# Kernel tuning notes

Hardware: AMD Instinct MI355X
Metric: run time of the kernel (lower is better)

## Reference

```python
import jax, jax.numpy as jnp
import numpy as np
from jax import lax

B, T, V, E, H, C = 16, 1024, 256, 512, 1024, 256


def lstm_layer(x, h0, c0, Wih, Whh, bih, bhh):
    """Single unidirectional LSTM layer, batch_first. x: (B,T,I). Returns (ys,(h,c)).
    Torch gate order: i, f, g, o. Input projection hoisted out of the scan (one big GEMM)."""
    xg = jnp.einsum('bti,gi->btg', x, Wih) + (bih + bhh)  # (B,T,4H)

    def step(carry, xt):
        h, c = carry
        gates = xt + h @ Whh.T
        i, f, g, o = jnp.split(gates, 4, axis=-1)
        c = jax.nn.sigmoid(f) * c + jax.nn.sigmoid(i) * jnp.tanh(g)
        h = jax.nn.sigmoid(o) * jnp.tanh(c)
        return (h, c), h

    (h, c), ys = lax.scan(step, (h0, c0), jnp.swapaxes(xg, 0, 1))
    return jnp.swapaxes(ys, 0, 1), h, c


def run_stack(emb_tokens, h0s, c0s, layers):
    """layers: list of (Wih, Whh, bih, bhh). h0s/c0s: (L,B,H)."""
    x = emb_tokens
    hs, cs = [], []
    for l, (Wih, Whh, bih, bhh) in enumerate(layers):
        x, h, c = lstm_layer(x, h0s[l], c0s[l], Wih, Whh, bih, bhh)
        hs.append(h)
        cs.append(c)
    return x, jnp.stack(hs), jnp.stack(cs)


def setup_inputs() -> dict:
    key = jax.random.key(0)
    ks = iter(jax.random.split(key, 32))
    s = 1.0 / np.sqrt(H)

    def u(shape):
        return jax.random.uniform(next(ks), shape, jnp.float32, -s, s)

    inp = {"x": jax.random.randint(next(ks), (B, T), 0, V)}
    inp["enc_emb"] = jax.random.normal(next(ks), (V, E), jnp.float32)
    inp["dec_emb"] = jax.random.normal(next(ks), (V, E), jnp.float32)
    for pre in ("enc", "dec"):
        for l in range(2):
            I = E if l == 0 else H
            inp[f"{pre}_Wih{l}"] = u((4 * H, I))
            inp[f"{pre}_Whh{l}"] = u((4 * H, H))
            inp[f"{pre}_bih{l}"] = u((4 * H,))
            inp[f"{pre}_bhh{l}"] = u((4 * H,))
    inp["out_W"] = u((C, H))
    inp["out_b"] = u((C,))
    return inp


def reference(x, enc_emb, dec_emb,
              enc_Wih0, enc_Whh0, enc_bih0, enc_bhh0,
              enc_Wih1, enc_Whh1, enc_bih1, enc_bhh1,
              dec_Wih0, dec_Whh0, dec_bih0, dec_bhh0,
              dec_Wih1, dec_Whh1, dec_bih1, dec_bhh1,
              out_W, out_b):
    enc_layers = [(enc_Wih0, enc_Whh0, enc_bih0, enc_bhh0),
                  (enc_Wih1, enc_Whh1, enc_bih1, enc_bhh1)]
    dec_layers = [(dec_Wih0, dec_Whh0, dec_bih0, dec_bhh0),
                  (dec_Wih1, dec_Whh1, dec_bih1, dec_bhh1)]
    L = len(enc_layers)
    z = jnp.zeros((L, x.shape[0], H), jnp.float32)
    # Encoder (dropout is identity at inference)
    _, h, c = run_stack(enc_emb[x], z, z, enc_layers)
    # Decoder with teacher forcing on the same tokens
    dec_out, _, _ = run_stack(dec_emb[x], h, c, dec_layers)
    logits = dec_out @ out_W.T + out_b  # (B,T,C)
    return jnp.swapaxes(logits, 1, 2)   # (B,C,T)
```

## Files before the change

### kernel.cpp

```cpp
#include <hip/hip_runtime.h>
#include <stdint.h>

#define B_  16
#define T_  1024
#define H_  1024
#define E_  512
#define V_  256
#define C_  256

typedef __bf16 bf16x8 __attribute__((ext_vector_type(8)));
typedef float  f32x4  __attribute__((ext_vector_type(4)));
typedef unsigned short u16;
typedef unsigned int   u32;
typedef unsigned long long u64;

__device__ __forceinline__ float bf2f(u16 u) {
  union { unsigned int i; float f; } v; v.i = ((unsigned int)u) << 16; return v.f;
}
__device__ __forceinline__ u16 f2bf(float f) {
  union { float f; unsigned int i; } v; v.f = f;
  unsigned int u = v.i;
  return (u16)((u + 0x7fffu + ((u >> 16) & 1u)) >> 16);
}
__device__ __forceinline__ bf16x8 ld_bf8(const u16* p) {
  uint4 v = *(const uint4*)p;
  return __builtin_bit_cast(bf16x8, v);
}
__device__ __forceinline__ bf16x8 ld_bf8_coh(const u16* p) {
  union { u64 q[2]; bf16x8 v; } r;
  r.q[0] = __hip_atomic_load((const u64*)p,     __ATOMIC_RELAXED, __HIP_MEMORY_SCOPE_AGENT);
  r.q[1] = __hip_atomic_load((const u64*)p + 1, __ATOMIC_RELAXED, __HIP_MEMORY_SCOPE_AGENT);
  return r.v;
}
__device__ __forceinline__ float sigm(float x) { return 1.f / (1.f + __expf(-x)); }
__device__ __forceinline__ float tanhfast(float x) {
  return 1.f - 2.f / (__expf(2.f * x) + 1.f);
}

__device__ __forceinline__ bf16x8 ldw8(const void* W, size_t off, bool f32in) {
  if (f32in) {
    const float* p = (const float*)W + off;
    float4 a = *(const float4*)p;
    float4 b = *(const float4*)(p + 4);
    union { u16 s[8]; bf16x8 v; } r;
    r.s[0]=f2bf(a.x); r.s[1]=f2bf(a.y); r.s[2]=f2bf(a.z); r.s[3]=f2bf(a.w);
    r.s[4]=f2bf(b.x); r.s[5]=f2bf(b.y); r.s[6]=f2bf(b.z); r.s[7]=f2bf(b.w);
    return r.v;
  }
  return ld_bf8((const u16*)W + off);
}
__device__ __forceinline__ float ldb1(const void* p, int i, bool f32in) {
  return f32in ? ((const float*)p)[i] : bf2f(((const u16*)p)[i]);
}

__global__ void probe_k(const u16* __restrict__ s, int* __restrict__ flag) {
  if (threadIdx.x == 0) {
    int cnt = 0;
    for (int i = 0; i < 256; ++i) {
      int e = (s[i] >> 7) & 0xFF;
      if (e >= 124) ++cnt;
    }
    flag[0] = (cnt >= 16) ? 1 : 0;
  }
}

__global__ void cvt_k(const void* __restrict__ src, u16* __restrict__ dst, int n,
                      const int* __restrict__ flagp) {
  int i = blockIdx.x * blockDim.x + threadIdx.x;
  if (i >= n) return;
  if (*flagp) dst[i] = f2bf(((const float*)src)[i]);
  else        dst[i] = ((const u16*)src)[i];
}

struct PersistArgs {
  const int* tok;
  const u16 *eemb, *demb;
  const void *Wih[4], *Whh[4], *bih[4], *bhh[4];
  u16 *zslot;
  u16 *he0[2], *he1[2], *hd0[2], *hd1[2];
  u16 *seq;
  u32 *flags;
  const int *dflag;
};

struct PhaseP {
  const void *Wx, *Wh, *bi, *bh;
  const u16* emb;
  const int* tok;
  u16 *r0[2], *r1[2];
  const u16 *h0init, *h1init;
  u16* seq;
  u32 *flags;
  bool f32in, init_c, last;
  int c0, bid, tid;
  u32 gp0;
};

__device__ __forceinline__ void gbar(u32* flags, int bid, int tid, u32 gp) {
  __syncthreads();
  if (tid == 0)
    __hip_atomic_store(&flags[bid * 16], gp, __ATOMIC_RELAXED, __HIP_MEMORY_SCOPE_AGENT);
  if (tid < 128) {
    while (__hip_atomic_load(&flags[tid * 16], __ATOMIC_RELAXED, __HIP_MEMORY_SCOPE_AGENT) < gp)
      __builtin_amdgcn_s_sleep(2);
  }
  __syncthreads();
}

template<int LAYER>
__device__ u32 run_phase(const PhaseP& q, f32x4* red4, float* gbuf, float* cbuf,
                         float* bbuf) {
  constexpr int KX = LAYER ? 1024 : 512;
  constexpr int NX = KX / 256;
  const int tid = q.tid, w = tid >> 6, l = tid & 63;
  const int rr = l & 15, ksub = (l >> 4) * 8;

  bf16x8 BX[4][NX], BH[4][4];
  #pragma unroll
  for (int g = 0; g < 4; ++g) {
    const size_t row = (size_t)(g * 1024 + q.c0 + rr);
    #pragma unroll
    for (int it = 0; it < NX; ++it)
      BX[g][it] = ldw8(q.Wx, row * KX + w * (KX / 8) + it * 32 + ksub, q.f32in);
    #pragma unroll
    for (int it = 0; it < 4; ++it)
      BH[g][it] = ldw8(q.Wh, row * 1024 + w * 128 + it * 32 + ksub, q.f32in);
  }
  if (tid < 64) {
    const int row = (tid >> 4) * 1024 + q.c0 + (tid & 15);
    bbuf[tid] = ldb1(q.bi, row, q.f32in) + ldb1(q.bh, row, q.f32in);
  }
  if (q.init_c && tid < 64) {
    #pragma unroll
    for (int k = 0; k < 4; ++k) cbuf[k * 64 + tid] = 0.f;
  }
  __syncthreads();

  int tok_cur = (LAYER == 0) ? q.tok[rr * T_ + 0] : 0;
  u32 gp = q.gp0;

  for (int s = 0; s <= T_; ++s) {
    const bool active = (LAYER == 0) ? (s < T_) : (s >= 1);
    if (active) {
      const u16* xrow;
      const u16* hrow;
      if (LAYER == 0) {
        xrow = q.emb + (size_t)tok_cur * 512;
        hrow = (s == 0) ? (q.h0init + rr * H_) : (q.r0[(s - 1) & 1] + rr * H_);
      } else {
        xrow = q.r0[(s - 1) & 1] + rr * H_;
        hrow = (s == 1) ? (q.h1init + rr * H_) : (q.r1[s & 1] + rr * H_);
      }
      bf16x8 ax[NX], ah[4];
      #pragma unroll
      for (int it = 0; it < NX; ++it)
        ax[it] = (LAYER == 0) ? ld_bf8(xrow + w * (KX / 8) + it * 32 + ksub)
                              : ld_bf8_coh(xrow + w * (KX / 8) + it * 32 + ksub);
      #pragma unroll
      for (int it = 0; it < 4; ++it)
        ah[it] = ld_bf8_coh(hrow + w * 128 + it * 32 + ksub);
      #pragma unroll
      for (int g = 0; g < 4; ++g) {
        f32x4 acc = {0.f, 0.f, 0.f, 0.f};
        #pragma unroll
        for (int it = 0; it < NX; ++it)
          acc = __builtin_amdgcn_mfma_f32_16x16x32_bf16(ax[it], BX[g][it], acc, 0, 0, 0);
        #pragma unroll
        for (int it = 0; it < 4; ++it)
          acc = __builtin_amdgcn_mfma_f32_16x16x32_bf16(ah[it], BH[g][it], acc, 0, 0, 0);
        red4[(w * 4 + g) * 64 + l] = acc;
      }
    }
    if (LAYER == 0) {
      const int tn = (s + 1 < T_) ? (s + 1) : (T_ - 1);
      tok_cur = q.tok[rr * T_ + tn];
    }
    __syncthreads();
    if (active && tid < 256) {
      const int g = tid >> 6, ll = tid & 63;
      f32x4 ssum = {0.f, 0.f, 0.f, 0.f};
      #pragma unroll
      for (int w8 = 0; w8 < 8; ++w8) ssum += red4[(w8 * 4 + g) * 64 + ll];
      const int n = ll & 15, mg = (ll >> 4) * 4;
      const float bsum = bbuf[g * 16 + n];
      #pragma unroll
      for (int r = 0; r < 4; ++r) gbuf[(g * 16 + n) * 17 + mg + r] = ssum[r] + bsum;
    }
    __syncthreads();
    if (active && tid < 64) {
      const int m = tid & 15, jg = tid >> 4;
      union { u16 s4[4]; u64 q8; } hp;
      #pragma unroll
      for (int k = 0; k < 4; ++k) {
        const int col = jg * 4 + k;
        const float iv = sigm(gbuf[( 0 + col) * 17 + m]);
        const float fv = sigm(gbuf[(16 + col) * 17 + m]);
        const float gv = tanhfast(gbuf[(32 + col) * 17 + m]);
        const float ov = sigm(gbuf[(48 + col) * 17 + m]);
        const float cn = fv * cbuf[k * 64 + tid] + iv * gv;
        cbuf[k * 64 + tid] = cn;
        hp.s4[k] = f2bf(ov * tanhfast(cn));
      }
      u16* outs = (LAYER == 0) ? q.r0[s & 1] : q.r1[(s - 1) & 1];
      __hip_atomic_store((u64*)(outs + m * H_ + q.c0 + jg * 4), hp.q8,
                         __ATOMIC_RELAXED, __HIP_MEMORY_SCOPE_AGENT);
      if (q.seq) {
        const int t = s - 1;
        *(u64*)(q.seq + ((size_t)m * T_ + t) * H_ + q.c0 + jg * 4) = hp.q8;
      }
    }
    if (q.last && s == T_) break;
    gbar(q.flags, q.bid, tid, gp);
    ++gp;
  }
  return gp;
}

__global__ __launch_bounds__(512, 2) void persist_k(PersistArgs P) {
  __shared__ f32x4 red4[32 * 64];
  __shared__ float gbuf[64 * 17];
  __shared__ float cbuf[4 * 64];
  __shared__ float bbuf[64];
  const int bid = blockIdx.x, tid = threadIdx.x;
  const int layer = bid >> 6;
  const int c0 = (bid & 63) * 16;
  const bool f32in = (*P.dflag != 0);

  u32 gp = 1;
  for (int ph = 0; ph < 2; ++ph) {
    PhaseP q;
    const int wi = ph * 2 + layer;
    q.Wx = P.Wih[wi]; q.Wh = P.Whh[wi]; q.bi = P.bih[wi]; q.bh = P.bhh[wi];
    q.emb = ph ? P.demb : P.eemb;
    q.tok = P.tok;
    q.r0[0] = ph ? P.hd0[0] : P.he0[0]; q.r0[1] = ph ? P.hd0[1] : P.he0[1];
    q.r1[0] = ph ? P.hd1[0] : P.he1[0]; q.r1[1] = ph ? P.hd1[1] : P.he1[1];
    q.h0init = ph ? P.he0[1] : P.zslot;
    q.h1init = ph ? P.he1[1] : P.zslot;
    q.seq = (ph == 1 && layer == 1) ? P.seq : nullptr;
    q.flags = P.flags;
    q.f32in = f32in; q.init_c = (ph == 0); q.last = (ph == 1);
    q.c0 = c0; q.bid = bid; q.tid = tid; q.gp0 = gp;
    gp = layer ? run_phase<1>(q, red4, gbuf, cbuf, bbuf)
               : run_phase<0>(q, red4, gbuf, cbuf, bbuf);
  }
}

__global__ __launch_bounds__(256) void logits_k(const u16* __restrict__ A,
                                                const u16* __restrict__ W,
                                                const u16* __restrict__ bias,
                                                void* __restrict__ out,
                                                const int* __restrict__ dflag) {
  const int wid  = blockIdx.x * 4 + (threadIdx.x >> 6);
  const int mt   = wid >> 4;
  const int nt   = wid & 15;
  const int lane = threadIdx.x & 63;
  const int l15  = lane & 15;
  const int quad = lane >> 4;
  const int ko   = quad * 8;
  const u16* arow = A + (size_t)(mt * 16 + l15) * H_;
  const u16* brow = W + (size_t)(nt * 16 + l15) * H_;
  f32x4 acc = {0.f,0.f,0.f,0.f};
  #pragma unroll 4
  for (int kk = 0; kk < H_; kk += 32) {
    acc = __builtin_amdgcn_mfma_f32_16x16x32_bf16(ld_bf8(arow + kk + ko),
                                                  ld_bf8(brow + kk + ko), acc, 0, 0, 0);
  }
  const int c  = nt * 16 + l15;
  const float bv = bf2f(bias[c]);
  const int f32out = *dflag;
  #pragma unroll
  for (int r = 0; r < 4; ++r) {
    const int m = mt * 16 + quad * 4 + r;
    const int b = m >> 10, t = m & 1023;
    const size_t idx = ((size_t)b * C_ + c) * T_ + t;
    const float v = acc[r] + bv;
    if (f32out) ((float*)out)[idx] = v;
    else        ((u16*)out)[idx]   = f2bf(v);
  }
}

extern "C" void kernel_launch(void* const* d_in, const int* in_sizes, int n_in,
                              void* d_out, int out_size, void* d_ws, size_t ws_size,
                              hipStream_t stream) {
  (void)in_sizes; (void)n_in; (void)out_size; (void)ws_size;

  const int* x = (const int*)d_in[0];

  char* ws = (char*)d_ws;
  u32* flags  = (u32*)ws;
  u16* zslot  = (u16*)(ws + 16384);
  int* dflag  = (int*)(ws + 49152);
  char* base  = ws + 49408;
  size_t ob = 0;
  u16* p_eemb = (u16*)(base + ob); ob += (size_t)V_ * E_ * 2;
  u16* p_demb = (u16*)(base + ob); ob += (size_t)V_ * E_ * 2;
  u16* p_outW = (u16*)(base + ob); ob += (size_t)C_ * H_ * 2;
  u16* p_outb = (u16*)(base + ob); ob += 512;
  u16* rings  = (u16*)(base + ob); ob += 8 * (size_t)B_ * H_ * 2;
  u16* seq    = (u16*)(base + ob); ob += (size_t)B_ * T_ * H_ * 2;
  const size_t SLOT = (size_t)B_ * H_;

  hipMemsetAsync(ws, 0, 49408, stream);

  probe_k<<<1, 64, 0, stream>>>((const u16*)d_in[5], dflag);

  cvt_k<<<(V_ * E_ + 255) / 256, 256, 0, stream>>>(d_in[1], p_eemb, V_ * E_, dflag);
  cvt_k<<<(V_ * E_ + 255) / 256, 256, 0, stream>>>(d_in[2], p_demb, V_ * E_, dflag);
  cvt_k<<<(C_ * H_ + 255) / 256, 256, 0, stream>>>(d_in[19], p_outW, C_ * H_, dflag);
  cvt_k<<<1, 256, 0, stream>>>(d_in[20], p_outb, C_, dflag);

  PersistArgs P;
  P.tok = x; P.eemb = p_eemb; P.demb = p_demb;
  for (int l = 0; l < 4; ++l) {
    P.Wih[l] = d_in[3 + 4 * l + 0];
    P.Whh[l] = d_in[3 + 4 * l + 1];
    P.bih[l] = d_in[3 + 4 * l + 2];
    P.bhh[l] = d_in[3 + 4 * l + 3];
  }
  P.zslot = zslot;
  P.he0[0] = rings + 0 * SLOT; P.he0[1] = rings + 1 * SLOT;
  P.he1[0] = rings + 2 * SLOT; P.he1[1] = rings + 3 * SLOT;
  P.hd0[0] = rings + 4 * SLOT; P.hd0[1] = rings + 5 * SLOT;
  P.hd1[0] = rings + 6 * SLOT; P.hd1[1] = rings + 7 * SLOT;
  P.seq = seq; P.flags = flags; P.dflag = dflag;

  persist_k<<<128, 512, 0, stream>>>(P);

  logits_k<<<4096, 256, 0, stream>>>(seq, p_outW, p_outb, d_out, dflag);
}
```

Baseline: 14.06 ms.

## Replace global barrier with tagged hidden-state polling and 4-deep rings

The all-block flag barrier that ran after every timestep is removed. Each bf16 hidden value is now stored in a 32-bit word with a step tag in the upper half. Consumers poll their input fragments until every tag matches the expected step, so each block waits only on the data it actually reads. The double-buffered rings become 4-slot rings, and layer 0 waits on a per-block layer-1 progress counter so it cannot overwrite slots still in use. This lets layer 0 run ahead of layer 1 and cuts barrier latency, at the cost of doubled ring traffic and busy polling on global memory.

```diff
diff --git a/kernel.cpp b/kernel.cpp
--- a/kernel.cpp
+++ b/kernel.cpp
@@ -26,11 +26,8 @@
   uint4 v = *(const uint4*)p;
   return __builtin_bit_cast(bf16x8, v);
 }
-__device__ __forceinline__ bf16x8 ld_bf8_coh(const u16* p) {
-  union { u64 q[2]; bf16x8 v; } r;
-  r.q[0] = __hip_atomic_load((const u64*)p,     __ATOMIC_RELAXED, __HIP_MEMORY_SCOPE_AGENT);
-  r.q[1] = __hip_atomic_load((const u64*)p + 1, __ATOMIC_RELAXED, __HIP_MEMORY_SCOPE_AGENT);
-  return r.v;
+__device__ __forceinline__ u64 ldq_coh(const u32* p) {
+  return __hip_atomic_load((const u64*)p, __ATOMIC_RELAXED, __HIP_MEMORY_SCOPE_AGENT);
 }
 __device__ __forceinline__ float sigm(float x) { return 1.f / (1.f + __expf(-x)); }
 __device__ __forceinline__ float tanhfast(float x) {
@@ -53,6 +50,36 @@
   return f32in ? ((const float*)p)[i] : bf2f(((const u16*)p)[i]);
 }
 
+template<int NF>
+__device__ __forceinline__ void poll_frags(const u32* row, int obase, u32 tag,
+                                           bf16x8* out) {
+  u64 q[NF * 4];
+  for (;;) {
+    #pragma unroll
+    for (int it = 0; it < NF; ++it) {
+      const u32* p = row + obase + it * 32;
+      q[it*4+0] = ldq_coh(p + 0); q[it*4+1] = ldq_coh(p + 2);
+      q[it*4+2] = ldq_coh(p + 4); q[it*4+3] = ldq_coh(p + 6);
+    }
+    u64 bad = 0;
+    #pragma unroll
+    for (int i = 0; i < NF * 4; ++i)
+      bad |= (((q[i] >> 16) & 0xffffu) ^ (u64)tag) | ((q[i] >> 48) ^ (u64)tag);
+    if (!bad) break;
+    __builtin_amdgcn_s_sleep(1);
+  }
+  #pragma unroll
+  for (int it = 0; it < NF; ++it) {
+    union { u32 w[4]; bf16x8 v; } r;
+    #pragma unroll
+    for (int j = 0; j < 4; ++j) {
+      const u64 qq = q[it*4+j];
+      r.w[j] = ((u32)qq & 0xffffu) | (((u32)(qq >> 32)) << 16);
+    }
+    out[it] = r.v;
+  }
+}
+
 __global__ void probe_k(const u16* __restrict__ s, int* __restrict__ flag) {
   if (threadIdx.x == 0) {
     int cnt = 0;
@@ -76,10 +103,10 @@
   const int* tok;
   const u16 *eemb, *demb;
   const void *Wih[4], *Whh[4], *bih[4], *bhh[4];
-  u16 *zslot;
-  u16 *he0[2], *he1[2], *hd0[2], *hd1[2];
+  const u32 *zslot;
+  u32 *he0, *he1, *hd0, *hd1;
   u16 *seq;
-  u32 *flags;
+  u32 *prog;
   const int *dflag;
 };
 
@@ -87,31 +114,21 @@
   const void *Wx, *Wh, *bi, *bh;
   const u16* emb;
   const int* tok;
-  u16 *r0[2], *r1[2];
-  const u16 *h0init, *h1init;
+  u32 *r0, *r1;
+  const u32 *h0init, *h1init;
   u16* seq;
-  u32 *flags;
-  bool f32in, init_c, last;
+  u32 *prog;
+  bool f32in, init_c;
   int c0, bid, tid;
-  u32 gp0;
+  u32 gbase;
 };
 
-__device__ __forceinline__ void gbar(u32* flags, int bid, int tid, u32 gp) {
-  __syncthreads();
-  if (tid == 0)
-    __hip_atomic_store(&flags[bid * 16], gp, __ATOMIC_RELAXED, __HIP_MEMORY_SCOPE_AGENT);
-  if (tid < 128) {
-    while (__hip_atomic_load(&flags[tid * 16], __ATOMIC_RELAXED, __HIP_MEMORY_SCOPE_AGENT) < gp)
-      __builtin_amdgcn_s_sleep(2);
-  }
-  __syncthreads();
-}
-
 template<int LAYER>
-__device__ u32 run_phase(const PhaseP& q, f32x4* red4, float* gbuf, float* cbuf,
-                         float* bbuf) {
+__device__ void run_phase(const PhaseP& q, f32x4* red4, float* gbuf, float* cbuf,
+                          float* bbuf) {
   constexpr int KX = LAYER ? 1024 : 512;
   constexpr int NX = KX / 256;
+  constexpr int SLOTN = 16 * 1024;
   const int tid = q.tid, w = tid >> 6, l = tid & 63;
   const int rr = l & 15, ksub = (l >> 4) * 8;
 
@@ -136,47 +153,51 @@
   }
   __syncthreads();
 
-  int tok_cur = (LAYER == 0) ? q.tok[rr * T_ + 0] : 0;
-  u32 gp = q.gp0;
-
-  for (int s = 0; s <= T_; ++s) {
-    const bool active = (LAYER == 0) ? (s < T_) : (s >= 1);
-    if (active) {
-      const u16* xrow;
-      const u16* hrow;
-      if (LAYER == 0) {
-        xrow = q.emb + (size_t)tok_cur * 512;
-        hrow = (s == 0) ? (q.h0init + rr * H_) : (q.r0[(s - 1) & 1] + rr * H_);
-      } else {
-        xrow = q.r0[(s - 1) & 1] + rr * H_;
-        hrow = (s == 1) ? (q.h1init + rr * H_) : (q.r1[s & 1] + rr * H_);
+  int tok_cur = LAYER ? 0 : q.tok[rr * T_];
+  const int s0 = LAYER ? 1 : 0;
+  const int s1 = LAYER ? T_ : T_ - 1;
+
+  for (int s = s0; s <= s1; ++s) {
+    bf16x8 ax[NX], ah[4];
+    if (LAYER == 0) {
+      const u16* xrow = q.emb + (size_t)tok_cur * 512;
+      #pragma unroll
+      for (int it = 0; it < NX; ++it)
+        ax[it] = ld_bf8(xrow + w * (KX / 8) + it * 32 + ksub);
+      const u32* hrow = (s == 0) ? (q.h0init + rr * H_)
+                                 : (q.r0 + ((s - 1) & 3) * SLOTN + rr * H_);
+      poll_frags<4>(hrow, w * 128 + ksub, q.gbase + (u32)s, ah);
+      if (s >= 4 && tid < 64) {
+        const u32 need = q.gbase + (u32)(s - 3);
+        while (__hip_atomic_load(&q.prog[tid * 16], __ATOMIC_RELAXED,
+                                 __HIP_MEMORY_SCOPE_AGENT) < need)
+          __builtin_amdgcn_s_sleep(8);
       }
-      bf16x8 ax[NX], ah[4];
+    } else {
+      const u32* xrow = q.r0 + ((s - 1) & 3) * SLOTN + rr * H_;
+      poll_frags<NX>(xrow, w * (KX / 8) + ksub, q.gbase + (u32)s, ax);
+      const u32* hrow = (s == 1) ? (q.h1init + rr * H_)
+                                 : (q.r1 + ((s - 2) & 3) * SLOTN + rr * H_);
+      poll_frags<4>(hrow, w * 128 + ksub, q.gbase + (u32)(s - 1), ah);
+    }
+    #pragma unroll
+    for (int g = 0; g < 4; ++g) {
+      f32x4 acc = {0.f, 0.f, 0.f, 0.f};
       #pragma unroll
       for (int it = 0; it < NX; ++it)
-        ax[it] = (LAYER == 0) ? ld_bf8(xrow + w * (KX / 8) + it * 32 + ksub)
-                              : ld_bf8_coh(xrow + w * (KX / 8) + it * 32 + ksub);
+        acc = __builtin_amdgcn_mfma_f32_16x16x32_bf16(ax[it], BX[g][it], acc, 0, 0, 0);
       #pragma unroll
       for (int it = 0; it < 4; ++it)
-        ah[it] = ld_bf8_coh(hrow + w * 128 + it * 32 + ksub);
-      #pragma unroll
-      for (int g = 0; g < 4; ++g) {
-        f32x4 acc = {0.f, 0.f, 0.f, 0.f};
-        #pragma unroll
-        for (int it = 0; it < NX; ++it)
-          acc = __builtin_amdgcn_mfma_f32_16x16x32_bf16(ax[it], BX[g][it], acc, 0, 0, 0);
-        #pragma unroll
-        for (int it = 0; it < 4; ++it)
-          acc = __builtin_amdgcn_mfma_f32_16x16x32_bf16(ah[it], BH[g][it], acc, 0, 0, 0);
-        red4[(w * 4 + g) * 64 + l] = acc;
-      }
-    }
-    if (LAYER == 0) {
-      const int tn = (s + 1 < T_) ? (s + 1) : (T_ - 1);
-      tok_cur = q.tok[rr * T_ + tn];
-    }
+        acc = __builtin_amdgcn_mfma_f32_16x16x32_bf16(ah[it], BH[g][it], acc, 0, 0, 0);
+      red4[(w * 4 + g) * 64 + l] = acc;
+    }
+    if (LAYER == 0)
+      tok_cur = q.tok[rr * T_ + ((s + 1 < T_) ? s + 1 : T_ - 1)];
     __syncthreads();
-    if (active && tid < 256) {
+    if (LAYER == 1 && tid == 0)
+      __hip_atomic_store(&q.prog[(q.bid & 63) * 16], q.gbase + (u32)s,
+                         __ATOMIC_RELAXED, __HIP_MEMORY_SCOPE_AGENT);
+    if (tid < 256) {
       const int g = tid >> 6, ll = tid & 63;
       f32x4 ssum = {0.f, 0.f, 0.f, 0.f};
       #pragma unroll
@@ -187,9 +208,10 @@
       for (int r = 0; r < 4; ++r) gbuf[(g * 16 + n) * 17 + mg + r] = ssum[r] + bsum;
     }
     __syncthreads();
-    if (active && tid < 64) {
+    if (tid < 64) {
       const int m = tid & 15, jg = tid >> 4;
-      union { u16 s4[4]; u64 q8; } hp;
+      const u32 stag = LAYER ? (q.gbase + (u32)s) : (q.gbase + (u32)(s + 1));
+      u32 wv[4];
       #pragma unroll
       for (int k = 0; k < 4; ++k) {
         const int col = jg * 4 + k;
@@ -199,21 +221,24 @@
         const float ov = sigm(gbuf[(48 + col) * 17 + m]);
         const float cn = fv * cbuf[k * 64 + tid] + iv * gv;
         cbuf[k * 64 + tid] = cn;
-        hp.s4[k] = f2bf(ov * tanhfast(cn));
+        wv[k] = (stag << 16) | (u32)f2bf(ov * tanhfast(cn));
       }
-      u16* outs = (LAYER == 0) ? q.r0[s & 1] : q.r1[(s - 1) & 1];
-      __hip_atomic_store((u64*)(outs + m * H_ + q.c0 + jg * 4), hp.q8,
+      u32* outs = LAYER ? (q.r1 + ((s - 1) & 3) * SLOTN)
+                        : (q.r0 + (s & 3) * SLOTN);
+      u64* dst = (u64*)(outs + (size_t)m * H_ + q.c0 + jg * 4);
+      __hip_atomic_store(dst,     (u64)wv[0] | ((u64)wv[1] << 32),
+                         __ATOMIC_RELAXED, __HIP_MEMORY_SCOPE_AGENT);
+      __hip_atomic_store(dst + 1, (u64)wv[2] | ((u64)wv[3] << 32),
                          __ATOMIC_RELAXED, __HIP_MEMORY_SCOPE_AGENT);
       if (q.seq) {
+        union { u16 s4[4]; u64 q8; } hp;
+        #pragma unroll
+        for (int k = 0; k < 4; ++k) hp.s4[k] = (u16)(wv[k] & 0xffffu);
         const int t = s - 1;
         *(u64*)(q.seq + ((size_t)m * T_ + t) * H_ + q.c0 + jg * 4) = hp.q8;
       }
     }
-    if (q.last && s == T_) break;
-    gbar(q.flags, q.bid, tid, gp);
-    ++gp;
-  }
-  return gp;
+  }
 }
 
 __global__ __launch_bounds__(512, 2) void persist_k(PersistArgs P) {
@@ -225,24 +250,25 @@
   const int layer = bid >> 6;
   const int c0 = (bid & 63) * 16;
   const bool f32in = (*P.dflag != 0);
-
-  u32 gp = 1;
+  constexpr int SLOTN = 16 * 1024;
+
   for (int ph = 0; ph < 2; ++ph) {
     PhaseP q;
     const int wi = ph * 2 + layer;
     q.Wx = P.Wih[wi]; q.Wh = P.Whh[wi]; q.bi = P.bih[wi]; q.bh = P.bhh[wi];
     q.emb = ph ? P.demb : P.eemb;
     q.tok = P.tok;
-    q.r0[0] = ph ? P.hd0[0] : P.he0[0]; q.r0[1] = ph ? P.hd0[1] : P.he0[1];
-    q.r1[0] = ph ? P.hd1[0] : P.he1[0]; q.r1[1] = ph ? P.hd1[1] : P.he1[1];
-    q.h0init = ph ? P.he0[1] : P.zslot;
-    q.h1init = ph ? P.he1[1] : P.zslot;
+    q.r0 = ph ? P.hd0 : P.he0;
+    q.r1 = ph ? P.hd1 : P.he1;
+    q.h0init = ph ? (P.he0 + 3 * SLOTN) : P.zslot;
+    q.h1init = ph ? (P.he1 + 3 * SLOTN) : P.zslot;
     q.seq = (ph == 1 && layer == 1) ? P.seq : nullptr;
-    q.flags = P.flags;
-    q.f32in = f32in; q.init_c = (ph == 0); q.last = (ph == 1);
-    q.c0 = c0; q.bid = bid; q.tid = tid; q.gp0 = gp;
-    gp = layer ? run_phase<1>(q, red4, gbuf, cbuf, bbuf)
-               : run_phase<0>(q, red4, gbuf, cbuf, bbuf);
+    q.prog = P.prog;
+    q.f32in = f32in; q.init_c = (ph == 0);
+    q.c0 = c0; q.bid = bid; q.tid = tid;
+    q.gbase = ph ? 1024u : 0u;
+    if (layer) run_phase<1>(q, red4, gbuf, cbuf, bbuf);
+    else       run_phase<0>(q, red4, gbuf, cbuf, bbuf);
   }
 }
 
@@ -288,20 +314,20 @@
   const int* x = (const int*)d_in[0];
 
   char* ws = (char*)d_ws;
-  u32* flags  = (u32*)ws;
-  u16* zslot  = (u16*)(ws + 16384);
-  int* dflag  = (int*)(ws + 49152);
-  char* base  = ws + 49408;
+  u32* prog   = (u32*)ws;
+  int* dflag  = (int*)(ws + 16384);
+  u32* zslot  = (u32*)(ws + 16640);
+  u32* rings  = (u32*)(ws + 82176);
+  char* base  = ws + 1130752;
   size_t ob = 0;
   u16* p_eemb = (u16*)(base + ob); ob += (size_t)V_ * E_ * 2;
   u16* p_demb = (u16*)(base + ob); ob += (size_t)V_ * E_ * 2;
   u16* p_outW = (u16*)(base + ob); ob += (size_t)C_ * H_ * 2;
   u16* p_outb = (u16*)(base + ob); ob += 512;
-  u16* rings  = (u16*)(base + ob); ob += 8 * (size_t)B_ * H_ * 2;
   u16* seq    = (u16*)(base + ob); ob += (size_t)B_ * T_ * H_ * 2;
-  const size_t SLOT = (size_t)B_ * H_;
-
-  hipMemsetAsync(ws, 0, 49408, stream);
+  const size_t RING = 4 * (size_t)16 * 1024;
+
+  hipMemsetAsync(ws, 0, 1130752, stream);
 
   probe_k<<<1, 64, 0, stream>>>((const u16*)d_in[5], dflag);
 
@@ -319,11 +345,11 @@
     P.bhh[l] = d_in[3 + 4 * l + 3];
   }
   P.zslot = zslot;
-  P.he0[0] = rings + 0 * SLOT; P.he0[1] = rings + 1 * SLOT;
-  P.he1[0] = rings + 2 * SLOT; P.he1[1] = rings + 3 * SLOT;
-  P.hd0[0] = rings + 4 * SLOT; P.hd0[1] = rings + 5 * SLOT;
-  P.hd1[0] = rings + 6 * SLOT; P.hd1[1] = rings + 7 * SLOT;
-  P.seq = seq; P.flags = flags; P.dflag = dflag;
+  P.he0 = rings + 0 * RING;
+  P.he1 = rings + 1 * RING;
+  P.hd0 = rings + 2 * RING;
+  P.hd1 = rings + 3 * RING;
+  P.seq = seq; P.prog = prog; P.dflag = dflag;
 
   persist_k<<<128, 512, 0, stream>>>(P);
 
```

Measured after the change: 27.57 ms. 96.1% more time.
